# Optimization experiments

Measured on AMD Instinct MI355X. Metric: run time of the kernel, lower is better.

The kernel has to match this reference:

```python
import jax, jax.numpy as jnp
import numpy as np
from jax import lax

BINS = 16
N_FFT = 2 * (BINS - 1)  # 30


def setup_inputs() -> dict:
    key = jax.random.key(0)
    k0, k1, k2, k3 = jax.random.split(key, 4)
    B, C, T = 16, 256, 8192
    c = C // BINS  # 16
    s = 1.0 / np.sqrt(C)  # keep attention logits in a sane range
    return {
        "x": jax.random.normal(k0, (B, C, T), dtype=jnp.float32),
        "Wk": jax.random.normal(k1, (c, C), dtype=jnp.float32) * s,
        "Wq": jax.random.normal(k2, (C, C), dtype=jnp.float32) * s,
        "Wv": jax.random.normal(k3, (C, C), dtype=jnp.float32) * s,
    }


def _spectrogram_power(sig):
    """torchaudio T.Spectrogram(n_fft=30, hop_length=1, normalized=True, power=2),
    implemented as a direct windowed-DFT conv (exact same math as the FFT).
    sig: [N, L] -> [N, BINS, L+1] frames (center=True, reflect pad)."""
    n = jnp.arange(N_FFT, dtype=jnp.float32)
    window = 0.5 - 0.5 * jnp.cos(2.0 * np.pi * n / N_FFT)  # periodic Hann
    kf = jnp.arange(BINS, dtype=jnp.float32)
    ang = 2.0 * np.pi * kf[:, None] * n[None, :] / N_FFT  # [BINS, N_FFT]
    # real and imaginary DFT kernels, window folded in: [2*BINS, N_FFT]
    dft = jnp.concatenate([jnp.cos(ang), -jnp.sin(ang)], axis=0) * window
    pad = N_FFT // 2
    sigp = jnp.pad(sig, ((0, 0), (pad, pad)), mode="reflect")[:, None, :]  # [N,1,L+30]
    spec = lax.conv_general_dilated(
        sigp, dft[:, None, :].astype(sig.dtype), (1,), "VALID",
        dimension_numbers=("NCH", "OIH", "NCH"))  # [N, 2*BINS, L+1]
    power = spec[:, :BINS, :] ** 2 + spec[:, BINS:, :] ** 2
    return power / jnp.sum(window ** 2)  # normalized=True -> / ||w||^2 on power


def reference(x, Wk, Wq, Wv):
    B, C, T = x.shape
    c = Wk.shape[0]
    xt = x.transpose(0, 2, 1)  # [B, T, C]
    k = jnp.einsum("btC,cC->bct", xt, Wk)   # [B, c, T]
    q = jnp.einsum("btC,cC->bct", xt, Wq)   # [B, C, T]
    v = jnp.einsum("btC,cC->bct", xt, Wv)   # [B, C, T]
    scores = jnp.einsum("bct,bCt->bcC", k, q) / (C ** 0.5)
    scores = jax.nn.softmax(scores, axis=-1)           # [B, c, C]
    out = jnp.einsum("bCt,bcC->bct", v, scores)        # [B, c, T]
    power = _spectrogram_power(out.reshape(B * c, T))  # [B*c, BINS, T+1]
    power = power[..., :T]                             # drop last frame ([:-1])
    return power.reshape(B, c * BINS, T)
```

## Files before the change

kernel.cpp:

```cpp
#include <hip/hip_runtime.h>
#include <math.h>

#define B_   16
#define C_   256
#define T_   8192
#define BINS 16
#define NFFT 30

typedef __attribute__((ext_vector_type(8))) _Float16 f16x8;
typedef __attribute__((ext_vector_type(2))) __fp16 fp16x2;
typedef __attribute__((ext_vector_type(4))) float f32x4;

typedef const __attribute__((address_space(1))) unsigned int ga_u32;
typedef __attribute__((address_space(3))) unsigned int ls_u32;

union f16pack { f16x8 v; fp16x2 p[4]; };

__global__ __launch_bounds__(512) void spec_tables(float* __restrict__ ctab,
                                                   float* __restrict__ stab) {
  const int i = threadIdx.x;
  if (i < BINS*NFFT) {
    const int k = i / NFFT, n = i % NFFT;
    const float TWO_PI = 6.283185307179586f;
    const float wn = 0.5f - 0.5f * cosf(TWO_PI * (float)n / (float)NFFT);
    const float ang = TWO_PI * (float)(k * n) / (float)NFFT;
    ctab[i] = cosf(ang) * wn;
    stab[i] = sinf(ang) * wn;
  }
}


static __device__ __forceinline__ void stage_panel(float* dstbase, const float* xb,
                                                   int koff, int tid) {
#pragma unroll
  for (int h = 0; h < 4; ++h) {
    const int idx = h*512 + tid;
    const int row = idx >> 3;
    const int ps  = idx & 7;
    const int ls  = ps ^ (row & 7);
    const float* src = xb + (size_t)row*T_ + koff + ls*4;
    __builtin_amdgcn_global_load_lds((ga_u32*)src, (ls_u32*)(dstbase + idx*4), 16, 0, 0);
  }
}

template<int NPT>
__global__ __launch_bounds__(512, 4) void gram_mfma(const float* __restrict__ x,
                                                    _Float16* __restrict__ gp) {
  const int ti = blockIdx.x;
  const int b  = blockIdx.y;
  const int ks = blockIdx.z;
  constexpr int KCH = T_ / NPT;

  __shared__ float P[2][256*32];

  const int tid  = threadIdx.x;
  const int lane = tid & 63;
  const int w    = tid >> 6;
  const int wr   = w >> 2;
  const int wc   = w & 3;
  const int fr   = lane & 15;
  const int g    = lane >> 4;

  const float* xb = x + ((size_t)b * C_) * T_;
  const int t0 = ks * KCH;

  f32x4 acc[4][4];
#pragma unroll
  for (int mt = 0; mt < 4; ++mt)
#pragma unroll
    for (int nt = 0; nt < 4; ++nt) acc[mt][nt] = (f32x4){0.f, 0.f, 0.f, 0.f};

  stage_panel(P[0], xb, t0, tid);
  __syncthreads();

  int cur = 0;
  for (int kt = 0; kt < KCH; kt += 32) {
    if (kt + 32 < KCH) stage_panel(P[cur ^ 1], xb, t0 + kt + 32, tid);

    const float* Pc = P[cur];
    f16pack fb[4];
#pragma unroll
    for (int nt = 0; nt < 4; ++nt) {
      const int r = wc*64 + nt*16 + fr;
      const float4 lo = *(const float4*)&Pc[r*32 + (((2*g+0) ^ (r&7))<<2)];
      const float4 hi = *(const float4*)&Pc[r*32 + (((2*g+1) ^ (r&7))<<2)];
      fb[nt].p[0] = __builtin_amdgcn_cvt_pkrtz(lo.x, lo.y);
      fb[nt].p[1] = __builtin_amdgcn_cvt_pkrtz(lo.z, lo.w);
      fb[nt].p[2] = __builtin_amdgcn_cvt_pkrtz(hi.x, hi.y);
      fb[nt].p[3] = __builtin_amdgcn_cvt_pkrtz(hi.z, hi.w);
    }
#pragma unroll
    for (int mt = 0; mt < 4; ++mt) {
      const int r = ti*128 + wr*64 + mt*16 + fr;
      const float4 lo = *(const float4*)&Pc[r*32 + (((2*g+0) ^ (r&7))<<2)];
      const float4 hi = *(const float4*)&Pc[r*32 + (((2*g+1) ^ (r&7))<<2)];
      f16pack fa;
      fa.p[0] = __builtin_amdgcn_cvt_pkrtz(lo.x, lo.y);
      fa.p[1] = __builtin_amdgcn_cvt_pkrtz(lo.z, lo.w);
      fa.p[2] = __builtin_amdgcn_cvt_pkrtz(hi.x, hi.y);
      fa.p[3] = __builtin_amdgcn_cvt_pkrtz(hi.z, hi.w);
#pragma unroll
      for (int nt = 0; nt < 4; ++nt)
        acc[mt][nt] = __builtin_amdgcn_mfma_f32_16x16x32_f16(fa.v, fb[nt].v, acc[mt][nt], 0, 0, 0);
    }
    __syncthreads();
    cur ^= 1;
  }

  _Float16* gpart = gp + ((size_t)(ks * 16 + b)) * 65536;
#pragma unroll
  for (int mt = 0; mt < 4; ++mt)
#pragma unroll
    for (int nt = 0; nt < 4; ++nt)
#pragma unroll
      for (int r = 0; r < 4; ++r) {
        const int gi = ti*128 + wr*64 + mt*16 + g*4 + r;
        const int gj = wc*64 + nt*16 + fr;
        gpart[(size_t)gi*256 + gj] = (_Float16)acc[mt][nt][r];
      }
}

template<int NPT>
__global__ __launch_bounds__(256) void attn_a_t(const float* __restrict__ Wk,
                                                const _Float16* __restrict__ gp,
                                                float* __restrict__ wkg) {
  const int tc = blockIdx.x;
  const int b  = blockIdx.y;
  const int tid = threadIdx.x;
  __shared__ float gl[256*32];

  const _Float16* g0 = gp + (size_t)b*65536 + tc*32;
#pragma unroll
  for (int i = 0; i < 32; ++i) {
    const int idx = i*256 + tid;
    const int r = idx >> 5, cl = idx & 31;
    const size_t off = (size_t)r*256 + cl;
    float s = 0.f;
#pragma unroll
    for (int p = 0; p < NPT; ++p) s += (float)g0[off + (size_t)p*1048576];
    gl[r*32 + cl] = s;
  }
  __syncthreads();

  const int cl  = tid & 31;
  const int cc0 = (tid >> 5) * 2;
#pragma unroll
  for (int h = 0; h < 2; ++h) {
    const int cc = cc0 + h;
    float a = 0.f;
    for (int c1 = 0; c1 < 256; c1 += 4) {
      const float4 w4 = *(const float4*)&Wk[cc*256 + c1];
      a += w4.x*gl[(c1+0)*32+cl] + w4.y*gl[(c1+1)*32+cl]
         + w4.z*gl[(c1+2)*32+cl] + w4.w*gl[(c1+3)*32+cl];
    }
    wkg[((size_t)b*16 + cc)*256 + tc*32 + cl] = a;
  }
}

__global__ __launch_bounds__(256) void attn_b(const float* __restrict__ Wq,
                                              const float* __restrict__ Wv,
                                              const float* __restrict__ wkg,
                                              float* __restrict__ Mout) {
  const int b = blockIdx.x;
  const int tid = threadIdx.x;
  __shared__ float s1[16*256];
  __shared__ float s2[16*256];
  __shared__ float invs[16];

#pragma unroll
  for (int cc = 0; cc < 16; ++cc) s1[cc*256 + tid] = wkg[((size_t)b*16 + cc)*256 + tid];
  __syncthreads();

  float sc[16];
#pragma unroll
  for (int cc = 0; cc < 16; ++cc) sc[cc] = 0.f;
  for (int c4 = 0; c4 < 64; ++c4) {
    const float4 wq4 = *(const float4*)&Wq[(size_t)tid*256 + c4*4];
#pragma unroll
    for (int cc = 0; cc < 16; ++cc) {
      const float4 p4 = *(const float4*)&s1[cc*256 + c4*4];
      sc[cc] += p4.x*wq4.x + p4.y*wq4.y + p4.z*wq4.z + p4.w*wq4.w;
    }
  }
#pragma unroll
  for (int cc = 0; cc < 16; ++cc) s2[cc*256 + tid] = sc[cc] * 0.0625f;
  __syncthreads();

  {
    const int rr = tid >> 4, jj = tid & 15;
    float mx = -1e30f;
    for (int c = jj; c < 256; c += 16) mx = fmaxf(mx, s2[rr*256 + c]);
    for (int o = 1; o < 16; o <<= 1) mx = fmaxf(mx, __shfl_xor(mx, o, 64));
    float sm = 0.f;
    for (int c = jj; c < 256; c += 16) {
      const float e = __expf(s2[rr*256 + c] - mx);
      s2[rr*256 + c] = e;
      sm += e;
    }
    for (int o = 1; o < 16; o <<= 1) sm += __shfl_xor(sm, o, 64);
    if (jj == 0) invs[rr] = 1.f / sm;
  }
  __syncthreads();

  float mac[16];
#pragma unroll
  for (int cc = 0; cc < 16; ++cc) mac[cc] = 0.f;
  for (int c4 = 0; c4 < 64; ++c4) {
    float wv[4];
#pragma unroll
    for (int j = 0; j < 4; ++j) wv[j] = Wv[(size_t)(c4*4 + j)*256 + tid];
#pragma unroll
    for (int cc = 0; cc < 16; ++cc) {
      const float4 p4 = *(const float4*)&s2[cc*256 + c4*4];
      mac[cc] += p4.x*wv[0] + p4.y*wv[1] + p4.z*wv[2] + p4.w*wv[3];
    }
  }
#pragma unroll
  for (int cc = 0; cc < 16; ++cc)
    Mout[(size_t)b*4096 + cc*256 + tid] = mac[cc] * invs[cc];
}

__global__ __launch_bounds__(256) void outp_kernel(const float* __restrict__ x,
                                                   const float* __restrict__ M,
                                                   float* __restrict__ seq) {
  const int tc = blockIdx.x;
  const int b  = blockIdx.y;
  const int tid = threadIdx.x;
  const int t  = tc*512 + tid*2;
  const float* xb = x + (size_t)b*C_*T_ + t;
  const float* mb = M + (size_t)b*4096;
  float2 a[16];
#pragma unroll
  for (int cc = 0; cc < 16; ++cc) a[cc] = make_float2(0.f, 0.f);
  for (int ch = 0; ch < 64; ++ch) {
    float2 xv[4];
#pragma unroll
    for (int j = 0; j < 4; ++j)
      xv[j] = *(const float2*)(xb + (size_t)(ch*4 + j) * T_);
#pragma unroll
    for (int cc = 0; cc < 16; ++cc) {
      const float4 m4 = *(const float4*)(mb + cc*256 + ch*4);
      a[cc].x += m4.x*xv[0].x + m4.y*xv[1].x + m4.z*xv[2].x + m4.w*xv[3].x;
      a[cc].y += m4.x*xv[0].y + m4.y*xv[1].y + m4.z*xv[2].y + m4.w*xv[3].y;
    }
  }
#pragma unroll
  for (int cc = 0; cc < 16; ++cc)
    *(float2*)(seq + (size_t)(b*16 + cc)*T_ + t) = a[cc];
}

__global__ __launch_bounds__(256) void spec_kernel(const float* __restrict__ seq,
                                                   const float* __restrict__ ctabg,
                                                   const float* __restrict__ stabg,
                                                   float* __restrict__ out) {
  const int tcx = blockIdx.x;
  const int r   = blockIdx.y;
  const int tid = threadIdx.x;
  const int t0  = tcx * 256;

  __shared__ float smem[288];
  __shared__ float ctab[BINS*NFFT];
  __shared__ float stab[BINS*NFFT];

  const float* row = seq + (size_t)r * T_;
  for (int i = tid; i < 288; i += 256) {
    int gg = t0 - 15 + i;
    if (gg < 0) gg = -gg;
    if (gg > T_-1) gg = 2*(T_-1) - gg;
    smem[i] = row[gg];
  }
  for (int i = tid; i < BINS*NFFT; i += 256) {
    ctab[i] = ctabg[i];
    stab[i] = stabg[i];
  }
  __syncthreads();

  const int k   = tid >> 4;
  const int sub = tid & 15;
  float cr[NFFT], ci[NFFT];
#pragma unroll
  for (int n = 0; n < NFFT; ++n) { cr[n] = ctab[k*NFFT + n]; ci[n] = stab[k*NFFT + n]; }

  float* orow = out + (size_t)(r*BINS + k) * T_ + t0;
  const float inv_norm = 1.0f / 11.25f;

  for (int jj = 0; jj < 4; ++jj) {
    const int x0 = 4*sub + 64*jj;
    float smp[36];
#pragma unroll
    for (int q = 0; q < 9; ++q) {
      const float4 v = *(const float4*)&smem[x0 + 4*q];
      smp[4*q+0] = v.x; smp[4*q+1] = v.y; smp[4*q+2] = v.z; smp[4*q+3] = v.w;
    }
    float4 pw;
#pragma unroll
    for (int p = 0; p < 4; ++p) {
      float re = 0.f, im = 0.f;
#pragma unroll
      for (int n = 0; n < NFFT; ++n) {
        re += cr[n] * smp[p + n];
        im += ci[n] * smp[p + n];
      }
      ((float*)&pw)[p] = (re*re + im*im) * inv_norm;
    }
    *(float4*)(orow + x0) = pw;
  }
}

extern "C" void kernel_launch(void* const* d_in, const int* in_sizes, int n_in,
                              void* d_out, int out_size, void* d_ws, size_t ws_size,
                              hipStream_t stream) {
  const float* x  = (const float*)d_in[0];
  const float* Wk = (const float*)d_in[1];
  const float* Wq = (const float*)d_in[2];
  const float* Wv = (const float*)d_in[3];
  float* out = (float*)d_out;
  float* ws  = (float*)d_ws;

  const size_t tail = 65536ull*2 + 2097152ull + 960ull;
  const int np = (ws_size >= (16ull*524288ull + tail) * 4ull) ? 16 : 8;

  _Float16* gp = (_Float16*)ws;
  float* fbase = ws + (size_t)np*524288;
  float* wkg  = fbase;
  float* M    = fbase + 65536;
  float* seq  = M + 65536;
  float* ctab = seq + 2097152;
  float* stab = ctab + 480;

  spec_tables<<<1, 512, 0, stream>>>(ctab, stab);
  if (np == 16) {
    gram_mfma<16><<<dim3(2, 16, 16), 512, 0, stream>>>(x, gp);
    attn_a_t<16><<<dim3(8, 16), 256, 0, stream>>>(Wk, gp, wkg);
  } else {
    gram_mfma<8><<<dim3(2, 16, 8), 512, 0, stream>>>(x, gp);
    attn_a_t<8><<<dim3(8, 16), 256, 0, stream>>>(Wk, gp, wkg);
  }
  attn_b<<<dim3(16), 256, 0, stream>>>(Wq, Wv, wkg, M);
  outp_kernel<<<dim3(16, 16), 256, 0, stream>>>(x, M, seq);
  spec_kernel<<<dim3(32, 256), 256, 0, stream>>>(seq, ctab, stab, out);
}
```

Before: 234.5 us.

## Replace full Gram matrix with k = Wk·x then R = k·xᵀ reduction

Instead of forming the full 256x256 Gram matrix x·xᵀ per batch and then multiplying by Wk, the code first computes k = Wk·x (16 rows) in a new kernel and stores it as fp16. It then computes R = k·xᵀ with MFMA over T chunks, writing fp32 partials that attn_b reduces. This cuts the MFMA work for the score stage by about 16x but adds a second full pass reading x and an extra kernel launch.

```diff
diff --git a/kernel.cpp b/kernel.cpp
--- a/kernel.cpp
+++ b/kernel.cpp
@@ -29,6 +29,31 @@
   }
 }
 
+__global__ __launch_bounds__(256) void k_kernel(const float* __restrict__ x,
+                                                const float* __restrict__ Wk,
+                                                _Float16* __restrict__ kk) {
+  const int tc = blockIdx.x;
+  const int b  = blockIdx.y;
+  const int tid = threadIdx.x;
+  const int t = tc*256 + tid;
+  const float* xb = x + (size_t)b*C_*T_ + t;
+  float acc[16];
+#pragma unroll
+  for (int cc = 0; cc < 16; ++cc) acc[cc] = 0.f;
+  for (int c4 = 0; c4 < 64; ++c4) {
+    float xv[4];
+#pragma unroll
+    for (int j = 0; j < 4; ++j) xv[j] = xb[(size_t)(c4*4 + j)*T_];
+#pragma unroll
+    for (int cc = 0; cc < 16; ++cc) {
+      const float4 w4 = *(const float4*)&Wk[cc*256 + c4*4];
+      acc[cc] += w4.x*xv[0] + w4.y*xv[1] + w4.z*xv[2] + w4.w*xv[3];
+    }
+  }
+#pragma unroll
+  for (int cc = 0; cc < 16; ++cc)
+    kk[((size_t)b*16 + cc)*T_ + t] = (_Float16)acc[cc];
+}
 
 static __device__ __forceinline__ void stage_panel(float* dstbase, const float* xb,
                                                    int koff, int tid) {
@@ -43,32 +68,28 @@
   }
 }
 
-template<int NPT>
-__global__ __launch_bounds__(512, 4) void gram_mfma(const float* __restrict__ x,
-                                                    _Float16* __restrict__ gp) {
-  const int ti = blockIdx.x;
+__global__ __launch_bounds__(512, 4) void r_kernel(const float* __restrict__ x,
+                                                   const _Float16* __restrict__ kk,
+                                                   float* __restrict__ Rp) {
+  const int ks = blockIdx.x;
   const int b  = blockIdx.y;
-  const int ks = blockIdx.z;
-  constexpr int KCH = T_ / NPT;
+  constexpr int KCH = 256;
 
   __shared__ float P[2][256*32];
 
   const int tid  = threadIdx.x;
   const int lane = tid & 63;
   const int w    = tid >> 6;
-  const int wr   = w >> 2;
-  const int wc   = w & 3;
   const int fr   = lane & 15;
   const int g    = lane >> 4;
 
-  const float* xb = x + ((size_t)b * C_) * T_;
+  const float* xb = x + (size_t)b*C_*T_;
+  const _Float16* kb = kk + (size_t)b*16*T_;
   const int t0 = ks * KCH;
 
-  f32x4 acc[4][4];
-#pragma unroll
-  for (int mt = 0; mt < 4; ++mt)
-#pragma unroll
-    for (int nt = 0; nt < 4; ++nt) acc[mt][nt] = (f32x4){0.f, 0.f, 0.f, 0.f};
+  f32x4 acc[2];
+  acc[0] = (f32x4){0.f,0.f,0.f,0.f};
+  acc[1] = (f32x4){0.f,0.f,0.f,0.f};
 
   stage_panel(P[0], xb, t0, tid);
   __syncthreads();
@@ -78,88 +99,37 @@
     if (kt + 32 < KCH) stage_panel(P[cur ^ 1], xb, t0 + kt + 32, tid);
 
     const float* Pc = P[cur];
-    f16pack fb[4];
-#pragma unroll
-    for (int nt = 0; nt < 4; ++nt) {
-      const int r = wc*64 + nt*16 + fr;
+    const f16x8 ka = *(const f16x8*)&kb[(size_t)fr*T_ + t0 + kt + g*8];
+#pragma unroll
+    for (int nt = 0; nt < 2; ++nt) {
+      const int r = (w*2 + nt)*16 + fr;
       const float4 lo = *(const float4*)&Pc[r*32 + (((2*g+0) ^ (r&7))<<2)];
       const float4 hi = *(const float4*)&Pc[r*32 + (((2*g+1) ^ (r&7))<<2)];
-      fb[nt].p[0] = __builtin_amdgcn_cvt_pkrtz(lo.x, lo.y);
-      fb[nt].p[1] = __builtin_amdgcn_cvt_pkrtz(lo.z, lo.w);
-      fb[nt].p[2] = __builtin_amdgcn_cvt_pkrtz(hi.x, hi.y);
-      fb[nt].p[3] = __builtin_amdgcn_cvt_pkrtz(hi.z, hi.w);
-    }
-#pragma unroll
-    for (int mt = 0; mt < 4; ++mt) {
-      const int r = ti*128 + wr*64 + mt*16 + fr;
-      const float4 lo = *(const float4*)&Pc[r*32 + (((2*g+0) ^ (r&7))<<2)];
-      const float4 hi = *(const float4*)&Pc[r*32 + (((2*g+1) ^ (r&7))<<2)];
-      f16pack fa;
-      fa.p[0] = __builtin_amdgcn_cvt_pkrtz(lo.x, lo.y);
-      fa.p[1] = __builtin_amdgcn_cvt_pkrtz(lo.z, lo.w);
-      fa.p[2] = __builtin_amdgcn_cvt_pkrtz(hi.x, hi.y);
-      fa.p[3] = __builtin_amdgcn_cvt_pkrtz(hi.z, hi.w);
-#pragma unroll
-      for (int nt = 0; nt < 4; ++nt)
-        acc[mt][nt] = __builtin_amdgcn_mfma_f32_16x16x32_f16(fa.v, fb[nt].v, acc[mt][nt], 0, 0, 0);
+      f16pack fb;
+      fb.p[0] = __builtin_amdgcn_cvt_pkrtz(lo.x, lo.y);
+      fb.p[1] = __builtin_amdgcn_cvt_pkrtz(lo.z, lo.w);
+      fb.p[2] = __builtin_amdgcn_cvt_pkrtz(hi.x, hi.y);
+      fb.p[3] = __builtin_amdgcn_cvt_pkrtz(hi.z, hi.w);
+      acc[nt] = __builtin_amdgcn_mfma_f32_16x16x32_f16(ka, fb.v, acc[nt], 0, 0, 0);
     }
     __syncthreads();
     cur ^= 1;
   }
 
-  _Float16* gpart = gp + ((size_t)(ks * 16 + b)) * 65536;
-#pragma unroll
-  for (int mt = 0; mt < 4; ++mt)
-#pragma unroll
-    for (int nt = 0; nt < 4; ++nt)
-#pragma unroll
-      for (int r = 0; r < 4; ++r) {
-        const int gi = ti*128 + wr*64 + mt*16 + g*4 + r;
-        const int gj = wc*64 + nt*16 + fr;
-        gpart[(size_t)gi*256 + gj] = (_Float16)acc[mt][nt][r];
-      }
-}
-
-template<int NPT>
-__global__ __launch_bounds__(256) void attn_a_t(const float* __restrict__ Wk,
-                                                const _Float16* __restrict__ gp,
-                                                float* __restrict__ wkg) {
-  const int tc = blockIdx.x;
-  const int b  = blockIdx.y;
-  const int tid = threadIdx.x;
-  __shared__ float gl[256*32];
-
-  const _Float16* g0 = gp + (size_t)b*65536 + tc*32;
-#pragma unroll
-  for (int i = 0; i < 32; ++i) {
-    const int idx = i*256 + tid;
-    const int r = idx >> 5, cl = idx & 31;
-    const size_t off = (size_t)r*256 + cl;
-    float s = 0.f;
-#pragma unroll
-    for (int p = 0; p < NPT; ++p) s += (float)g0[off + (size_t)p*1048576];
-    gl[r*32 + cl] = s;
-  }
-  __syncthreads();
-
-  const int cl  = tid & 31;
-  const int cc0 = (tid >> 5) * 2;
-#pragma unroll
-  for (int h = 0; h < 2; ++h) {
-    const int cc = cc0 + h;
-    float a = 0.f;
-    for (int c1 = 0; c1 < 256; c1 += 4) {
-      const float4 w4 = *(const float4*)&Wk[cc*256 + c1];
-      a += w4.x*gl[(c1+0)*32+cl] + w4.y*gl[(c1+1)*32+cl]
-         + w4.z*gl[(c1+2)*32+cl] + w4.w*gl[(c1+3)*32+cl];
-    }
-    wkg[((size_t)b*16 + cc)*256 + tc*32 + cl] = a;
-  }
+  float* rp = Rp + ((size_t)(ks*16 + b))*4096;
+#pragma unroll
+  for (int nt = 0; nt < 2; ++nt)
+#pragma unroll
+    for (int r = 0; r < 4; ++r) {
+      const int cc = g*4 + r;
+      const int ch = (w*2 + nt)*16 + fr;
+      rp[cc*256 + ch] = acc[nt][r];
+    }
 }
 
 __global__ __launch_bounds__(256) void attn_b(const float* __restrict__ Wq,
                                               const float* __restrict__ Wv,
-                                              const float* __restrict__ wkg,
+                                              const float* __restrict__ Rp,
                                               float* __restrict__ Mout) {
   const int b = blockIdx.x;
   const int tid = threadIdx.x;
@@ -168,7 +138,13 @@
   __shared__ float invs[16];
 
 #pragma unroll
-  for (int cc = 0; cc < 16; ++cc) s1[cc*256 + tid] = wkg[((size_t)b*16 + cc)*256 + tid];
+  for (int cc = 0; cc < 16; ++cc) {
+    float s = 0.f;
+#pragma unroll 8
+    for (int p = 0; p < 32; ++p)
+      s += Rp[((size_t)(p*16 + b))*4096 + cc*256 + tid];
+    s1[cc*256 + tid] = s;
+  }
   __syncthreads();
 
   float sc[16];
@@ -317,26 +293,17 @@
   float* out = (float*)d_out;
   float* ws  = (float*)d_ws;
 
-  const size_t tail = 65536ull*2 + 2097152ull + 960ull;
-  const int np = (ws_size >= (16ull*524288ull + tail) * 4ull) ? 16 : 8;
-
-  _Float16* gp = (_Float16*)ws;
-  float* fbase = ws + (size_t)np*524288;
-  float* wkg  = fbase;
-  float* M    = fbase + 65536;
+  _Float16* kk = (_Float16*)ws;
+  float* Rp   = ws + 1048576;
+  float* M    = Rp + 2097152;
   float* seq  = M + 65536;
   float* ctab = seq + 2097152;
   float* stab = ctab + 480;
 
   spec_tables<<<1, 512, 0, stream>>>(ctab, stab);
-  if (np == 16) {
-    gram_mfma<16><<<dim3(2, 16, 16), 512, 0, stream>>>(x, gp);
-    attn_a_t<16><<<dim3(8, 16), 256, 0, stream>>>(Wk, gp, wkg);
-  } else {
-    gram_mfma<8><<<dim3(2, 16, 8), 512, 0, stream>>>(x, gp);
-    attn_a_t<8><<<dim3(8, 16), 256, 0, stream>>>(Wk, gp, wkg);
-  }
-  attn_b<<<dim3(16), 256, 0, stream>>>(Wq, Wv, wkg, M);
+  k_kernel<<<dim3(32, 16), 256, 0, stream>>>(x, Wk, kk);
+  r_kernel<<<dim3(32, 16), 512, 0, stream>>>(x, kk, Rp);
+  attn_b<<<dim3(16), 256, 0, stream>>>(Wq, Wv, Rp, M);
   outp_kernel<<<dim3(16, 16), 256, 0, stream>>>(x, M, seq);
   spec_kernel<<<dim3(32, 256), 256, 0, stream>>>(seq, ctab, stab, out);
 }
```

Measured after the change: 232.4 us. About the same (-0.9%).
